# Kernel optimization log

Hardware: AMD Instinct MI355X
Metric: run time of the kernel (lower is better)

## Reference

```python
import jax, jax.numpy as jnp
import numpy as np

N, E, F_IN, EDIM, HEADS, DIM = 100000, 1600000, 128, 16, 4, 16
HC = HEADS * DIM


def add_self_loops_mean(src, dst, ea, n):
    # PyG add_self_loops with fill_value='mean': self-loop edge_attr is the mean
    # of incoming-edge attrs per target node (0 for isolated nodes).
    cnt = jax.ops.segment_sum(jnp.ones((dst.shape[0],), ea.dtype), dst, num_segments=n)
    sm = jax.ops.segment_sum(ea, dst, num_segments=n)
    loop = jnp.where(cnt[:, None] > 0, sm / jnp.maximum(cnt, 1.0)[:, None], 0.0)
    idx = jnp.arange(n, dtype=src.dtype)
    return (jnp.concatenate([src, idx]), jnp.concatenate([dst, idx]),
            jnp.concatenate([ea, loop], axis=0))


def gatv2(x, src, dst, ea, Wl, bl, Wr, br, We, att, bias):
    n = x.shape[0]
    h, c = att.shape
    xl = (x @ Wl + bl).reshape(n, h, c)   # source transform (lin_l)
    xr = (x @ Wr + br).reshape(n, h, c)   # target transform (lin_r)
    ee = (ea @ We).reshape(-1, h, c)      # edge transform (lin_edge, no bias)
    s = jax.nn.leaky_relu(xl[src] + xr[dst] + ee, negative_slope=0.2)  # [E,h,c]
    alpha = jnp.einsum('ehc,hc->eh', s, att)                           # [E,h]
    amax = jax.ops.segment_max(alpha, dst, num_segments=n)
    amax = jnp.where(jnp.isfinite(amax), amax, 0.0)
    ex = jnp.exp(alpha - amax[dst])
    denom = jax.ops.segment_sum(ex, dst, num_segments=n)
    a = ex / (denom[dst] + 1e-16)                                      # segment softmax
    out = jax.ops.segment_sum(xl[src] * a[:, :, None], dst, num_segments=n)
    return out.reshape(n, h * c) + bias


def setup_inputs() -> dict:
    key = jax.random.key(0)
    ks = jax.random.split(key, 24)
    s = 0.1
    d = {
        'x': jax.random.normal(ks[0], (N, F_IN), jnp.float32),
        'edge_index': jax.random.randint(ks[1], (2, E), 0, N, jnp.int32),
        'edge_attr': jax.random.normal(ks[2], (E, EDIM), jnp.float32),
        'Wl1': jax.random.normal(ks[3], (F_IN, HC)) * s, 'bl1': jnp.zeros((HC,)),
        'Wr1': jax.random.normal(ks[4], (F_IN, HC)) * s, 'br1': jnp.zeros((HC,)),
        'We1': jax.random.normal(ks[5], (EDIM, HC)) * s,
        'att1': jax.random.normal(ks[6], (HEADS, DIM)) * s,
        'bias1': jnp.zeros((HC,)),
        'Wl2': jax.random.normal(ks[7], (HC, HC)) * s, 'bl2': jnp.zeros((HC,)),
        'Wr2': jax.random.normal(ks[8], (HC, HC)) * s, 'br2': jnp.zeros((HC,)),
        'We2': jax.random.normal(ks[9], (EDIM, HC)) * s,
        'att2': jax.random.normal(ks[10], (HEADS, DIM)) * s,
        'bias2': jnp.zeros((HC,)),
        'W_lin1': jax.random.normal(ks[11], (HC, DIM)) * s, 'b_lin1': jnp.zeros((DIM,)),
        'W_lin2': jax.random.normal(ks[12], (DIM, 1)) * s, 'b_lin2': jnp.zeros((1,)),
    }
    return d


def reference(x, edge_index, edge_attr, Wl1, bl1, Wr1, br1, We1, att1, bias1,
              Wl2, bl2, Wr2, br2, We2, att2, bias2,
              W_lin1, b_lin1, W_lin2, b_lin2):
    src, dst, ea = add_self_loops_mean(edge_index[0], edge_index[1], edge_attr, x.shape[0])
    h = jax.nn.relu(gatv2(x, src, dst, ea, Wl1, bl1, Wr1, br1, We1, att1, bias1))
    h = jax.nn.relu(gatv2(h, src, dst, ea, Wl2, bl2, Wr2, br2, We2, att2, bias2))
    h = jax.nn.relu(h @ W_lin1 + b_lin1)
    # dropout p=0.1 is identity in eval mode
    out = jax.nn.sigmoid((h @ W_lin2 + b_lin2)[:, 0])
    return out
```

## Files before the change

kernel.cpp:

```cpp
#include <hip/hip_runtime.h>
#include <stdint.h>

typedef unsigned short u16;
typedef unsigned int u32;
typedef unsigned long long u64;

typedef __attribute__((ext_vector_type(8))) short bfrag;
typedef __attribute__((ext_vector_type(4))) float f32x4;
typedef __attribute__((ext_vector_type(2))) float f32x2;

__device__ __forceinline__ float bf2f(u16 u) { return __uint_as_float(((u32)u) << 16); }
__device__ __forceinline__ u16 f2bf(float f) {
    u32 i = __float_as_uint(f);
    u32 r = i + 0x7fffu + ((i >> 16) & 1u);
    return (u16)(r >> 16);
}
__device__ __forceinline__ float lo16(u32 u) { return __uint_as_float(u << 16); }
__device__ __forceinline__ float hi16(u32 u) { return __uint_as_float(u & 0xffff0000u); }
__device__ __forceinline__ u32 pack2(float a, float b) {
    return (u32)f2bf(a) | ((u32)f2bf(b) << 16);
}
#define RFL(x) __builtin_amdgcn_readfirstlane(x)

#define DPP_ROR_ADD(p, ctrl) \
    p += __int_as_float(__builtin_amdgcn_update_dpp(0, __float_as_int(p), ctrl, 0xF, 0xF, false))
__device__ __forceinline__ float red16(float p) {
    DPP_ROR_ADD(p, 0x128);
    DPP_ROR_ADD(p, 0x124);
    DPP_ROR_ADD(p, 0x122);
    DPP_ROR_ADD(p, 0x121);
    return p;
}

__global__ void deg_hist(const int* __restrict__ dst, int E, int* __restrict__ deg) {
    int e = blockIdx.x * blockDim.x + threadIdx.x;
    if (e < E) atomicAdd(&deg[dst[e]], 1);
}

#define SCAN_T 256
#define SCAN_E 8
#define SCAN_CHUNK 2048

__global__ void scan_partial(const int* __restrict__ deg, int n, int* __restrict__ partials) {
    __shared__ int sh[SCAN_T];
    int b = blockIdx.x, t = threadIdx.x;
    int base = b * SCAN_CHUNK + t * SCAN_E;
    int s = 0;
#pragma unroll
    for (int i = 0; i < SCAN_E; i++) { int idx = base + i; if (idx < n) s += deg[idx]; }
    sh[t] = s; __syncthreads();
    for (int off = SCAN_T / 2; off > 0; off >>= 1) {
        if (t < off) sh[t] += sh[t + off];
        __syncthreads();
    }
    if (t == 0) partials[b] = sh[0];
}

__global__ void scan_mid(int* __restrict__ partials, int nb) {
    if (threadIdx.x == 0 && blockIdx.x == 0) {
        int acc = 0;
        for (int i = 0; i < nb; i++) { int v = partials[i]; partials[i] = acc; acc += v; }
    }
}

__global__ void scan_final(const int* __restrict__ deg, int n, const int* __restrict__ partials,
                           int* __restrict__ offs, int E) {
    __shared__ int sh[SCAN_T];
    int b = blockIdx.x, t = threadIdx.x;
    int base = b * SCAN_CHUNK + t * SCAN_E;
    int loc[SCAN_E];
    int s = 0;
#pragma unroll
    for (int i = 0; i < SCAN_E; i++) {
        int idx = base + i;
        int v = (idx < n) ? deg[idx] : 0;
        loc[i] = s; s += v;
    }
    sh[t] = s; __syncthreads();
    for (int off = 1; off < SCAN_T; off <<= 1) {
        int v = 0;
        if (t >= off) v = sh[t - off];
        __syncthreads();
        if (t >= off) sh[t] += v;
        __syncthreads();
    }
    int tbase = partials[b] + sh[t] - s;
#pragma unroll
    for (int i = 0; i < SCAN_E; i++) { int idx = base + i; if (idx < n) offs[idx] = tbase + loc[i]; }
    if (b == gridDim.x - 1 && t == SCAN_T - 1) offs[n] = E;
}

__global__ void csr_fill_split(const int* __restrict__ srcv, const int* __restrict__ dstv,
                               const float4* __restrict__ ea, int E,
                               int* __restrict__ cursor,
                               int* __restrict__ csrc, float4* __restrict__ cattr) {
    int e = blockIdx.x * blockDim.x + threadIdx.x;
    if (e >= E) return;
    const float4* s = ea + (u64)e * 4;
    float4 v0 = s[0], v1 = s[1], v2 = s[2], v3 = s[3];
    int sr = srcv[e];
    int d = dstv[e];
    int p = atomicAdd(&cursor[d], 1);
    csrc[p] = sr;
    float4* dp = cattr + (u64)p * 4;
    dp[0] = v0; dp[1] = v1; dp[2] = v2; dp[3] = v3;
}

template <int K>
__global__ void pack_w(const float* __restrict__ Wl, const float* __restrict__ Wr,
                       u32* __restrict__ Wb) {
    constexpr int NKS = K / 32;
    int t = blockIdx.x * blockDim.x + threadIdx.x;
    if (t >= 8 * NKS * 64) return;
    int lane = t & 63;
    int ks = (t >> 6) % NKS;
    int ct = (t >> 6) / NKS;
    int n = lane & 15, quad = lane >> 4;
    int c = ct * 16 + n;
    const float* W = (c < 64) ? Wl : Wr;
    int cc = c & 63;
    u32* d = Wb + (u64)t * 4;
#pragma unroll
    for (int p = 0; p < 4; p++) {
        int k0 = ks * 32 + quad * 8 + 2 * p;
        d[p] = pack2(W[(u64)k0 * 64 + cc], W[(u64)(k0 + 1) * 64 + cc]);
    }
}

template <int K, bool XF32>
__global__ __launch_bounds__(256) void gemm_mfma(const void* __restrict__ Xv,
                                                 const u32* __restrict__ Wb,
                                                 const float* __restrict__ bl,
                                                 const float* __restrict__ br,
                                                 int N, u16* __restrict__ xl, u16* __restrict__ xr) {
    constexpr int NKS = K / 32;
    int lane = threadIdx.x & 63;
    int gw = (blockIdx.x * 256 + threadIdx.x) >> 6;
    int row0 = gw * 16;
    if (row0 >= N) return;
    int m = lane & 15, quad = lane >> 4;

    f32x4 acc[8];
#pragma unroll
    for (int ct = 0; ct < 8; ct++) acc[ct] = (f32x4){0.f, 0.f, 0.f, 0.f};

#pragma unroll
    for (int ks = 0; ks < NKS; ks++) {
        bfrag a;
        if (XF32) {
            const float* xp = (const float*)Xv + (u64)(row0 + m) * K + ks * 32 + quad * 8;
            float4 v0 = *(const float4*)xp;
            float4 v1 = *(const float4*)(xp + 4);
            union { bfrag v; u32 d[4]; } au;
            au.d[0] = pack2(v0.x, v0.y); au.d[1] = pack2(v0.z, v0.w);
            au.d[2] = pack2(v1.x, v1.y); au.d[3] = pack2(v1.z, v1.w);
            a = au.v;
        } else {
            a = *(const bfrag*)((const u16*)Xv + (u64)(row0 + m) * K + ks * 32 + quad * 8);
        }
#pragma unroll
        for (int ct = 0; ct < 8; ct++) {
            bfrag b = *(const bfrag*)(Wb + (u64)((ct * NKS + ks) * 64 + lane) * 4);
            acc[ct] = __builtin_amdgcn_mfma_f32_16x16x32_bf16(a, b, acc[ct], 0, 0, 0);
        }
    }

#pragma unroll
    for (int ct = 0; ct < 8; ct++) {
        float bv = (ct < 4) ? bl[ct * 16 + m] : br[(ct - 4) * 16 + m];
        u16* dbuf = (ct < 4) ? xl : xr;
        int cc = (ct & 3) * 16 + m;
#pragma unroll
        for (int r = 0; r < 4; r++) {
            int row = row0 + quad * 4 + r;
            dbuf[(u64)row * 64 + cc] = f2bf(acc[ct][r] + bv);
        }
    }
}

__global__ __launch_bounds__(256) void gat_layer(const u16* __restrict__ xl, const u16* __restrict__ xr,
                                                 const int* __restrict__ offs,
                                                 const int* __restrict__ csrc,
                                                 const float* __restrict__ cattr,
                                                 const float* __restrict__ We,
                                                 const float* __restrict__ att,
                                                 const float* __restrict__ bias,
                                                 int N, u16* __restrict__ out) {
    int l = threadIdx.x & 63;
    int wid = RFL((int)((blockIdx.x * 256 + threadIdx.x) >> 6));
    int nw = gridDim.x * 4;
    f32x2 wec2[8];
#pragma unroll
    for (int k = 0; k < 8; k++) {
        wec2[k].x = We[(2 * k) * 64 + l];
        wec2[k].y = We[(2 * k + 1) * 64 + l];
    }
    float att_ls = att[l] * 1.44269504088896340736f;
    float bias_l = bias[l];

    for (int n = wid; n < N; n += nw) {
        float xr_l = bf2f(xr[(u32)(n * 64 + l)]);
        float xl_self = bf2f(xl[(u32)(n * 64 + l)]);
        int a = RFL(offs[n]);
        int b = RFL(offs[n + 1]);

        float lsum0 = 0.f, lsum1 = 0.f, o0 = 0.f, o1 = 0.f, es0 = 0.f, es1 = 0.f;

        auto edge_c = [&](const float* eap, float xlv, float& lsum, float& o, float& eesum) {
            f32x2 e0 = {0.f, 0.f}, e1 = {0.f, 0.f};
#pragma unroll
            for (int k = 0; k < 4; k++) {
                f32x2 a0 = *(const f32x2*)(eap + 4 * k);
                f32x2 a1 = *(const f32x2*)(eap + 4 * k + 2);
                e0 = __builtin_elementwise_fma(a0, wec2[2 * k], e0);
                e1 = __builtin_elementwise_fma(a1, wec2[2 * k + 1], e1);
            }
            f32x2 es = e0 + e1;
            float eef = es.x + es.y;
            eesum += eef;
            float z = (eef + xr_l) + xlv;
            z = fmaxf(z, 0.2f * z);
            float vv = red16(z * att_ls);
            float w;
            asm("v_exp_f32 %0, %1" : "=v"(w) : "v"(vv));
            lsum += w;
            o = fmaf(w, xlv, o);
        };

        for (int base = a; base < b; base += 64) {
            int rem = b - base;
            int cnt = rem < 64 ? rem : 64;
            int idx = base + l;
            int sv = csrc[idx < b ? idx : (b - 1)];
            int j = 0;
            for (; j + 4 <= cnt; j += 4) {
                int s0 = __builtin_amdgcn_readlane(sv, j);
                int s1 = __builtin_amdgcn_readlane(sv, j + 1);
                int s2 = __builtin_amdgcn_readlane(sv, j + 2);
                int s3 = __builtin_amdgcn_readlane(sv, j + 3);
                float xlv0 = bf2f(xl[(u32)(s0 * 64 + l)]);
                float xlv1 = bf2f(xl[(u32)(s1 * 64 + l)]);
                float xlv2 = bf2f(xl[(u32)(s2 * 64 + l)]);
                float xlv3 = bf2f(xl[(u32)(s3 * 64 + l)]);
                const float* ep = cattr + (u64)(base + j) * 16;
                edge_c(ep,      xlv0, lsum0, o0, es0);
                edge_c(ep + 16, xlv1, lsum1, o1, es1);
                edge_c(ep + 32, xlv2, lsum0, o0, es0);
                edge_c(ep + 48, xlv3, lsum1, o1, es1);
            }
            for (; j < cnt; j++) {
                int s0 = __builtin_amdgcn_readlane(sv, j);
                float xlv0 = bf2f(xl[(u32)(s0 * 64 + l)]);
                edge_c(cattr + (u64)(base + j) * 16, xlv0, lsum0, o0, es0);
            }
        }

        float lsum = lsum0 + lsum1;
        float o = o0 + o1;
        float eesum = es0 + es1;

        {
            int deg = b - a;
            float inv = (deg > 0) ? 1.f / (float)deg : 0.f;
            float z = (eesum * inv + xr_l) + xl_self;
            z = fmaxf(z, 0.2f * z);
            float vv = red16(z * att_ls);
            float w;
            asm("v_exp_f32 %0, %1" : "=v"(w) : "v"(vv));
            lsum += w;
            o = fmaf(w, xl_self, o);
        }

        float res = o / (lsum + 1e-16f) + bias_l;
        res = fmaxf(res, 0.f);
        out[(u32)(n * 64 + l)] = f2bf(res);
    }
}

__global__ __launch_bounds__(256) void mlp_head(const u16* __restrict__ h,
                                                const float* __restrict__ W1, const float* __restrict__ b1,
                                                const float* __restrict__ W2, const float* __restrict__ b2,
                                                int N, float* __restrict__ out) {
    __shared__ float w1[64 * 16];
    __shared__ float sb1[16];
    __shared__ float w2[16];
    for (int i = threadIdx.x; i < 64 * 16; i += 256) w1[i] = W1[i];
    if (threadIdx.x < 16) { sb1[threadIdx.x] = b1[threadIdx.x]; w2[threadIdx.x] = W2[threadIdx.x]; }
    __syncthreads();
    float b2v = b2[0];
    int n = blockIdx.x * blockDim.x + threadIdx.x;
    if (n < N) {
        float hv[64];
        const u32* hp = (const u32*)(h + (u64)n * 64);
#pragma unroll
        for (int i = 0; i < 32; i++) { u32 u = hp[i]; hv[2 * i] = lo16(u); hv[2 * i + 1] = hi16(u); }
        float z = b2v;
        for (int j = 0; j < 16; j++) {
            float acc = sb1[j];
#pragma unroll
            for (int k = 0; k < 64; k++) acc = fmaf(hv[k], w1[k * 16 + j], acc);
            acc = fmaxf(acc, 0.f);
            z = fmaf(acc, w2[j], z);
        }
        out[n] = 1.f / (1.f + __expf(-z));
    }
}

extern "C" void kernel_launch(void* const* d_in, const int* in_sizes, int n_in,
                              void* d_out, int out_size, void* d_ws, size_t ws_size,
                              hipStream_t stream) {
    const float* x    = (const float*)d_in[0];
    const int*   ei   = (const int*)d_in[1];
    const float* ea   = (const float*)d_in[2];
    const float* Wl1  = (const float*)d_in[3];
    const float* bl1  = (const float*)d_in[4];
    const float* Wr1  = (const float*)d_in[5];
    const float* br1  = (const float*)d_in[6];
    const float* We1  = (const float*)d_in[7];
    const float* att1 = (const float*)d_in[8];
    const float* bias1= (const float*)d_in[9];
    const float* Wl2  = (const float*)d_in[10];
    const float* bl2  = (const float*)d_in[11];
    const float* Wr2  = (const float*)d_in[12];
    const float* br2  = (const float*)d_in[13];
    const float* We2  = (const float*)d_in[14];
    const float* att2 = (const float*)d_in[15];
    const float* bias2= (const float*)d_in[16];
    const float* W1   = (const float*)d_in[17];
    const float* b1   = (const float*)d_in[18];
    const float* W2   = (const float*)d_in[19];
    const float* b2   = (const float*)d_in[20];
    float* out = (float*)d_out;

    const int N = in_sizes[0] / 128;
    const int E = in_sizes[1] / 2;
    const int* srcv = ei;
    const int* dstv = ei + E;

    uint8_t* p = (uint8_t*)d_ws;
    auto carve = [&](size_t bytes) -> void* {
        void* r = (void*)p;
        p += (bytes + 255) & ~(size_t)255;
        return r;
    };
    int*  deg     = (int*)carve((size_t)N * 4);
    int*  cursor  = (int*)carve((size_t)N * 4);
    int*  offs    = (int*)carve((size_t)(N + 1) * 4);
    int*  partials= (int*)carve(4096);
    int*  csrc    = (int*)carve((size_t)E * 4);
    float* cattr  = (float*)carve((size_t)E * 64);
    u16*  xl      = (u16*)carve((size_t)N * 64 * 2);
    u16*  xr      = (u16*)carve((size_t)N * 64 * 2);
    u16*  hb      = (u16*)carve((size_t)N * 64 * 2);
    u32*  wb1     = (u32*)carve(8 * 4 * 64 * 16);
    u32*  wb2     = (u32*)carve(8 * 2 * 64 * 16);
    (void)ws_size; (void)n_in; (void)out_size;

    hipMemsetAsync(deg, 0, (size_t)N * 4, stream);

    const int B = 256;
    pack_w<128><<<8, 256, 0, stream>>>(Wl1, Wr1, wb1);
    pack_w<64><<<4, 256, 0, stream>>>(Wl2, Wr2, wb2);

    deg_hist<<<(E + B - 1) / B, B, 0, stream>>>(dstv, E, deg);
    int nb = (N + SCAN_CHUNK - 1) / SCAN_CHUNK;
    scan_partial<<<nb, SCAN_T, 0, stream>>>(deg, N, partials);
    scan_mid<<<1, 64, 0, stream>>>(partials, nb);
    scan_final<<<nb, SCAN_T, 0, stream>>>(deg, N, partials, offs, E);
    hipMemcpyAsync(cursor, offs, (size_t)N * 4, hipMemcpyDeviceToDevice, stream);
    csr_fill_split<<<(E + B - 1) / B, B, 0, stream>>>(srcv, dstv, (const float4*)ea, E,
                                                      cursor, csrc, (float4*)cattr);

    int gemm_blocks = (N / 16 + 3) / 4;
    gemm_mfma<128, true><<<gemm_blocks, 256, 0, stream>>>(x, wb1, bl1, br1, N, xl, xr);
    gat_layer<<<8192, 256, 0, stream>>>(xl, xr, offs, csrc, cattr,
                                        We1, att1, bias1, N, hb);
    gemm_mfma<64, false><<<gemm_blocks, 256, 0, stream>>>(hb, wb2, bl2, br2, N, xl, xr);
    gat_layer<<<8192, 256, 0, stream>>>(xl, xr, offs, csrc, cattr,
                                        We2, att2, bias2, N, hb);
    mlp_head<<<(N + B - 1) / B, B, 0, stream>>>(hb, W1, b1, W2, b2, N, out);
}
```

Before: 640.3 us.

## Stop permuting edge attributes into CSR; gather them by edge index instead

The histogram kernel now records each edge's rank within its destination, so CSR fill becomes a plain scatter of (src, edge id) pairs. This removes the cursor copy and the 64-byte-per-edge attribute permutation. The GAT kernel instead gathers edge attributes from the original array through the stored edge id, so these reads are now random rather than contiguous, in both layers. The 4-edge inner loop is also interleaved so the four DPP reductions and exps run together for more ILP.

```diff
diff --git a/kernel.cpp b/kernel.cpp
--- a/kernel.cpp
+++ b/kernel.cpp
@@ -32,9 +32,10 @@
     return p;
 }
 
-__global__ void deg_hist(const int* __restrict__ dst, int E, int* __restrict__ deg) {
+__global__ void rank_hist(const int* __restrict__ dst, int E,
+                          int* __restrict__ deg, int* __restrict__ rank) {
     int e = blockIdx.x * blockDim.x + threadIdx.x;
-    if (e < E) atomicAdd(&deg[dst[e]], 1);
+    if (e < E) rank[e] = atomicAdd(&deg[dst[e]], 1);
 }
 
 #define SCAN_T 256
@@ -90,20 +91,15 @@
     if (b == gridDim.x - 1 && t == SCAN_T - 1) offs[n] = E;
 }
 
-__global__ void csr_fill_split(const int* __restrict__ srcv, const int* __restrict__ dstv,
-                               const float4* __restrict__ ea, int E,
-                               int* __restrict__ cursor,
-                               int* __restrict__ csrc, float4* __restrict__ cattr) {
+__global__ void csr_fill_idx(const int* __restrict__ srcv, const int* __restrict__ dstv,
+                             const int* __restrict__ rank,
+                             const int* __restrict__ offs, int E,
+                             int2* __restrict__ cse) {
     int e = blockIdx.x * blockDim.x + threadIdx.x;
     if (e >= E) return;
-    const float4* s = ea + (u64)e * 4;
-    float4 v0 = s[0], v1 = s[1], v2 = s[2], v3 = s[3];
-    int sr = srcv[e];
     int d = dstv[e];
-    int p = atomicAdd(&cursor[d], 1);
-    csrc[p] = sr;
-    float4* dp = cattr + (u64)p * 4;
-    dp[0] = v0; dp[1] = v1; dp[2] = v2; dp[3] = v3;
+    int p = offs[d] + rank[e];
+    cse[p] = make_int2(srcv[e], e);
 }
 
 template <int K>
@@ -180,8 +176,8 @@
 
 __global__ __launch_bounds__(256) void gat_layer(const u16* __restrict__ xl, const u16* __restrict__ xr,
                                                  const int* __restrict__ offs,
-                                                 const int* __restrict__ csrc,
-                                                 const float* __restrict__ cattr,
+                                                 const int2* __restrict__ cse,
+                                                 const float* __restrict__ ea,
                                                  const float* __restrict__ We,
                                                  const float* __restrict__ att,
                                                  const float* __restrict__ bias,
@@ -206,7 +202,7 @@
 
         float lsum0 = 0.f, lsum1 = 0.f, o0 = 0.f, o1 = 0.f, es0 = 0.f, es1 = 0.f;
 
-        auto edge_c = [&](const float* eap, float xlv, float& lsum, float& o, float& eesum) {
+        auto edge_1 = [&](const float* eap, float xlv, float& lsum, float& o, float& eesum) {
             f32x2 e0 = {0.f, 0.f}, e1 = {0.f, 0.f};
 #pragma unroll
             for (int k = 0; k < 4; k++) {
@@ -231,27 +227,70 @@
             int rem = b - base;
             int cnt = rem < 64 ? rem : 64;
             int idx = base + l;
-            int sv = csrc[idx < b ? idx : (b - 1)];
+            int2 sev = cse[idx < b ? idx : (b - 1)];
+            int sv = sev.x, ev = sev.y;
             int j = 0;
             for (; j + 4 <= cnt; j += 4) {
                 int s0 = __builtin_amdgcn_readlane(sv, j);
                 int s1 = __builtin_amdgcn_readlane(sv, j + 1);
                 int s2 = __builtin_amdgcn_readlane(sv, j + 2);
                 int s3 = __builtin_amdgcn_readlane(sv, j + 3);
+                int e0i = __builtin_amdgcn_readlane(ev, j);
+                int e1i = __builtin_amdgcn_readlane(ev, j + 1);
+                int e2i = __builtin_amdgcn_readlane(ev, j + 2);
+                int e3i = __builtin_amdgcn_readlane(ev, j + 3);
                 float xlv0 = bf2f(xl[(u32)(s0 * 64 + l)]);
                 float xlv1 = bf2f(xl[(u32)(s1 * 64 + l)]);
                 float xlv2 = bf2f(xl[(u32)(s2 * 64 + l)]);
                 float xlv3 = bf2f(xl[(u32)(s3 * 64 + l)]);
-                const float* ep = cattr + (u64)(base + j) * 16;
-                edge_c(ep,      xlv0, lsum0, o0, es0);
-                edge_c(ep + 16, xlv1, lsum1, o1, es1);
-                edge_c(ep + 32, xlv2, lsum0, o0, es0);
-                edge_c(ep + 48, xlv3, lsum1, o1, es1);
+                const float* ep[4] = { ea + (u64)e0i * 16, ea + (u64)e1i * 16,
+                                       ea + (u64)e2i * 16, ea + (u64)e3i * 16 };
+                f32x2 p0[4], p1[4];
+#pragma unroll
+                for (int u = 0; u < 4; u++) { p0[u] = (f32x2){0.f, 0.f}; p1[u] = (f32x2){0.f, 0.f}; }
+#pragma unroll
+                for (int k = 0; k < 4; k++) {
+#pragma unroll
+                    for (int u = 0; u < 4; u++) {
+                        f32x2 a0 = *(const f32x2*)(ep[u] + 4 * k);
+                        f32x2 a1 = *(const f32x2*)(ep[u] + 4 * k + 2);
+                        p0[u] = __builtin_elementwise_fma(a0, wec2[2 * k], p0[u]);
+                        p1[u] = __builtin_elementwise_fma(a1, wec2[2 * k + 1], p1[u]);
+                    }
+                }
+                float xlv[4] = {xlv0, xlv1, xlv2, xlv3};
+                float zz[4], eef[4];
+#pragma unroll
+                for (int u = 0; u < 4; u++) {
+                    f32x2 es = p0[u] + p1[u];
+                    eef[u] = es.x + es.y;
+                    float z = (eef[u] + xr_l) + xlv[u];
+                    z = fmaxf(z, 0.2f * z);
+                    zz[u] = z * att_ls;
+                }
+                es0 += eef[0] + eef[2];
+                es1 += eef[1] + eef[3];
+#define R4(ctrl) { DPP_ROR_ADD(zz[0], ctrl); DPP_ROR_ADD(zz[1], ctrl); \
+                   DPP_ROR_ADD(zz[2], ctrl); DPP_ROR_ADD(zz[3], ctrl); }
+                R4(0x128) R4(0x124) R4(0x122) R4(0x121)
+#undef R4
+                float w0, w1, w2, w3;
+                asm("v_exp_f32 %0, %1" : "=v"(w0) : "v"(zz[0]));
+                asm("v_exp_f32 %0, %1" : "=v"(w1) : "v"(zz[1]));
+                asm("v_exp_f32 %0, %1" : "=v"(w2) : "v"(zz[2]));
+                asm("v_exp_f32 %0, %1" : "=v"(w3) : "v"(zz[3]));
+                lsum0 += w0 + w2;
+                lsum1 += w1 + w3;
+                o0 = fmaf(w0, xlv0, o0);
+                o1 = fmaf(w1, xlv1, o1);
+                o0 = fmaf(w2, xlv2, o0);
+                o1 = fmaf(w3, xlv3, o1);
             }
             for (; j < cnt; j++) {
                 int s0 = __builtin_amdgcn_readlane(sv, j);
+                int e0i = __builtin_amdgcn_readlane(ev, j);
                 float xlv0 = bf2f(xl[(u32)(s0 * 64 + l)]);
-                edge_c(cattr + (u64)(base + j) * 16, xlv0, lsum0, o0, es0);
+                edge_1(ea + (u64)e0i * 16, xlv0, lsum0, o0, es0);
             }
         }
 
@@ -344,11 +383,10 @@
         return r;
     };
     int*  deg     = (int*)carve((size_t)N * 4);
-    int*  cursor  = (int*)carve((size_t)N * 4);
+    int*  rank    = (int*)carve((size_t)E * 4);
     int*  offs    = (int*)carve((size_t)(N + 1) * 4);
     int*  partials= (int*)carve(4096);
-    int*  csrc    = (int*)carve((size_t)E * 4);
-    float* cattr  = (float*)carve((size_t)E * 64);
+    int2* cse     = (int2*)carve((size_t)E * 8);
     u16*  xl      = (u16*)carve((size_t)N * 64 * 2);
     u16*  xr      = (u16*)carve((size_t)N * 64 * 2);
     u16*  hb      = (u16*)carve((size_t)N * 64 * 2);
@@ -362,21 +400,19 @@
     pack_w<128><<<8, 256, 0, stream>>>(Wl1, Wr1, wb1);
     pack_w<64><<<4, 256, 0, stream>>>(Wl2, Wr2, wb2);
 
-    deg_hist<<<(E + B - 1) / B, B, 0, stream>>>(dstv, E, deg);
+    rank_hist<<<(E + B - 1) / B, B, 0, stream>>>(dstv, E, deg, rank);
     int nb = (N + SCAN_CHUNK - 1) / SCAN_CHUNK;
     scan_partial<<<nb, SCAN_T, 0, stream>>>(deg, N, partials);
     scan_mid<<<1, 64, 0, stream>>>(partials, nb);
     scan_final<<<nb, SCAN_T, 0, stream>>>(deg, N, partials, offs, E);
-    hipMemcpyAsync(cursor, offs, (size_t)N * 4, hipMemcpyDeviceToDevice, stream);
-    csr_fill_split<<<(E + B - 1) / B, B, 0, stream>>>(srcv, dstv, (const float4*)ea, E,
-                                                      cursor, csrc, (float4*)cattr);
+    csr_fill_idx<<<(E + B - 1) / B, B, 0, stream>>>(srcv, dstv, rank, offs, E, cse);
 
     int gemm_blocks = (N / 16 + 3) / 4;
     gemm_mfma<128, true><<<gemm_blocks, 256, 0, stream>>>(x, wb1, bl1, br1, N, xl, xr);
-    gat_layer<<<8192, 256, 0, stream>>>(xl, xr, offs, csrc, cattr,
+    gat_layer<<<8192, 256, 0, stream>>>(xl, xr, offs, cse, ea,
                                         We1, att1, bias1, N, hb);
     gemm_mfma<64, false><<<gemm_blocks, 256, 0, stream>>>(hb, wb2, bl2, br2, N, xl, xr);
-    gat_layer<<<8192, 256, 0, stream>>>(xl, xr, offs, csrc, cattr,
+    gat_layer<<<8192, 256, 0, stream>>>(xl, xr, offs, cse, ea,
                                         We2, att2, bias2, N, hb);
     mlp_head<<<(N + B - 1) / B, B, 0, stream>>>(hb, W1, b1, W2, b2, N, out);
 }
```

New measurement: 624.6 us. 1.03x faster.
